# Kernel tuning notes

Measured on AMD Instinct MI355X. Metric: run time of the kernel, lower is better.

The kernel has to match this reference:

```python
import math
import jax, jax.numpy as jnp
import numpy as np

NUM_HEADS = 8
HEAD_DIM = 64


def setup_inputs() -> dict:
    key = jax.random.key(0)
    k1, k2, k3, k4 = jax.random.split(key, 4)
    C = 256
    E = NUM_HEADS * HEAD_DIM  # 512
    x = jax.random.normal(k1, (4, C, 48, 48), dtype=jnp.float32)
    Wqkv = jax.random.normal(k2, (3 * E, C), dtype=jnp.float32) * (1.0 / math.sqrt(C))
    Wout = jax.random.normal(k3, (C, E), dtype=jnp.float32) * (1.0 / math.sqrt(E))
    bout = jax.random.normal(k4, (C,), dtype=jnp.float32) * 0.01
    return {"x": x, "Wqkv": Wqkv, "Wout": Wout, "bout": bout}


def reference(x, Wqkv, Wout, bout):
    b, c, H, W = x.shape
    nh, hd = NUM_HEADS, HEAD_DIM
    N = H * W
    scale = 1.0 / math.sqrt(hd)
    # 1x1 conv (no bias) == channel matmul
    qkv = jnp.einsum('bcxy,oc->boxy', x, Wqkv)            # [b, 3*nh*hd, H, W]
    qkv = qkv.reshape(b, 3, nh, hd, N)                    # channel split order: (k, h, d)
    q, k, v = qkv[:, 0], qkv[:, 1], qkv[:, 2]             # each [b, nh, hd, N]
    att = jnp.einsum('bhdi,bhdj->bhij', q, k) * scale     # [b, nh, N, N]
    att = jax.nn.softmax(att, axis=-1)                    # stable (max-subtract inside)
    out = jnp.einsum('bhij,bhdj->bhid', att, v)           # [b, nh, N, hd]
    out = out.transpose(0, 1, 3, 2).reshape(b, nh * hd, H, W)  # 'b h (x y) d -> b (h d) x y'
    # 1x1 conv with bias
    return jnp.einsum('bexy,ce->bcxy', out, Wout) + bout[None, :, None, None]
```

## Files before the change

### kernel.cpp

```cpp
#include <hip/hip_runtime.h>

typedef __attribute__((ext_vector_type(8))) __bf16 bf16x8;
typedef __attribute__((ext_vector_type(16))) float f32x16;
typedef __attribute__((ext_vector_type(4))) float f32x4;
typedef __attribute__((ext_vector_type(4))) unsigned short us4;

__device__ __forceinline__ unsigned short f2bf(float f) {
  __bf16 h = (__bf16)f;
  return __builtin_bit_cast(unsigned short, h);
}
__device__ __forceinline__ unsigned pack2bf(float lo, float hi) {
  return (unsigned)f2bf(lo) | ((unsigned)f2bf(hi) << 16);
}

#define GLL(src, dst)                                                            \
  __builtin_amdgcn_global_load_lds((const __attribute__((address_space(1))) void*)(src), \
                                   (__attribute__((address_space(3))) void*)(dst), 16, 0, 0)

__device__ __forceinline__ void stage_chunks(const unsigned short* g, int ld,
                                             unsigned short* lds, int rows, int tid) {
  int total = rows * 8;
  for (int c0 = 0; c0 < total; c0 += 256) {
    int c = c0 + tid;
    int row = c >> 3, kc = c & 7;
    const unsigned short* src = g + (size_t)row * ld + ((kc ^ (row & 7)) << 3);
    unsigned short* dst = lds + (size_t)(c0 + (tid & 192)) * 8;
    GLL(src, dst);
  }
}

__device__ __forceinline__ bf16x8 frag(const unsigned short* lds, int row, int kc) {
  return *(const bf16x8*)(lds + row * 64 + ((kc ^ (row & 7)) << 3));
}


__global__ void k_cvt(const float* __restrict__ in, unsigned short* __restrict__ outp, int n) {
  int i = (blockIdx.x * 256 + threadIdx.x) * 4;
  if (i + 3 < n) {
    f32x4 v = *(const f32x4*)(in + i);
    us4 o;
#pragma unroll
    for (int k = 0; k < 4; k++) o[k] = f2bf(v[k]);
    *(us4*)(outp + i) = o;
  }
}

__global__ __launch_bounds__(256) void k_xpose(const float* __restrict__ x,
                                               unsigned short* __restrict__ xT) {
  __shared__ float t[32][33];
  int tid = threadIdx.x;
  int col = tid & 31, rowb = tid >> 5;
  int nt = blockIdx.x * 32, ct = blockIdx.y * 32, b = blockIdx.z;
  const float* src = x + ((size_t)b * 256 + ct) * 2304 + nt;
#pragma unroll
  for (int rr = 0; rr < 32; rr += 8) t[rowb + rr][col] = src[(size_t)(rowb + rr) * 2304 + col];
  __syncthreads();
  unsigned short* dst = xT + ((size_t)b * 2304 + nt) * 256 + ct;
#pragma unroll
  for (int rr = 0; rr < 32; rr += 8) dst[(size_t)(rowb + rr) * 256 + col] = f2bf(t[col][rowb + rr]);
}

__global__ __launch_bounds__(256, 2) void k_gemm_qkv(
    const unsigned short* __restrict__ W, const unsigned short* __restrict__ xT,
    unsigned short* __restrict__ qT, unsigned short* __restrict__ kT,
    unsigned short* __restrict__ vv) {
  __shared__ unsigned short As[128 * 64];
  __shared__ unsigned short Bs[128 * 64];
  int tid = threadIdx.x, lane = tid & 63, wid = tid >> 6;
  int m0 = blockIdx.x * 128, n0 = blockIdx.y * 128, b = blockIdx.z;
  const unsigned short* Ag = W + (size_t)m0 * 256;
  const unsigned short* Bg = xT + ((size_t)b * 2304 + n0) * 256;
  int wm = (wid >> 1) * 64, wn = (wid & 1) * 64;
  f32x4 acc[4][4] = {};
  for (int kt = 0; kt < 256; kt += 64) {
    __syncthreads();
    stage_chunks(Ag + kt, 256, As, 128, tid);
    stage_chunks(Bg + kt, 256, Bs, 128, tid);
    __syncthreads();
#pragma unroll
    for (int kk = 0; kk < 2; kk++) {
      bf16x8 af[4], bf[4];
#pragma unroll
      for (int i = 0; i < 4; i++) af[i] = frag(As, wm + i * 16 + (lane & 15), kk * 4 + (lane >> 4));
#pragma unroll
      for (int j = 0; j < 4; j++) bf[j] = frag(Bs, wn + j * 16 + (lane & 15), kk * 4 + (lane >> 4));
#pragma unroll
      for (int i = 0; i < 4; i++)
#pragma unroll
        for (int j = 0; j < 4; j++)
          acc[i][j] = __builtin_amdgcn_mfma_f32_16x16x32_bf16(af[i], bf[j], acc[i][j], 0, 0, 0);
    }
  }
#pragma unroll
  for (int i = 0; i < 4; i++) {
    int o = m0 + wm + i * 16 + ((lane >> 4) << 2);
    int which = o >> 9, h = (o >> 6) & 7, d0 = o & 63;
#pragma unroll
    for (int j = 0; j < 4; j++) {
      int n = n0 + wn + j * 16 + (lane & 15);
      if (which == 2) {
#pragma unroll
        for (int jj = 0; jj < 4; jj++)
          vv[((size_t)(b * 8 + h) * 64 + d0 + jj) * 2304 + n] = f2bf(acc[i][j][jj]);
      } else {
        float sc = which ? 1.0f : 0.18033688011112042f;
        us4 pk;
#pragma unroll
        for (int jj = 0; jj < 4; jj++) pk[jj] = f2bf(acc[i][j][jj] * sc);
        unsigned short* dst = (which ? kT : qT) + ((size_t)(b * 8 + h) * 2304 + n) * 64 + d0;
        *(us4*)dst = pk;
      }
    }
  }
}

__global__ __launch_bounds__(256, 4) void k_attn(
    const unsigned short* __restrict__ qT, const unsigned short* __restrict__ kT,
    const unsigned short* __restrict__ vv, unsigned short* __restrict__ o2T) {
  __shared__ unsigned short L[2][2][4096];
  int tid = threadIdx.x, lane = tid & 63;
  int wid = tid >> 6, rh = wid & 1, jh = wid >> 1;
  int il = lane & 31, g = lane >> 5;
  int lin = blockIdx.x;
  int xcd = lin & 7, idx = lin >> 3;
  int bh = xcd * 4 + idx / 36;
  int i0 = (idx % 36) * 64;
  const unsigned short* kT_bh = kT + (size_t)bh * 2304 * 64;
  const unsigned short* vv_bh = vv + (size_t)bh * 64 * 2304;
  const unsigned short* qrow = qT + ((size_t)bh * 2304 + i0 + rh * 32 + il) * 64;
  bf16x8 qf[4];
#pragma unroll
  for (int ks = 0; ks < 4; ks++) qf[ks] = *(const bf16x8*)(qrow + (ks * 2 + g) * 8);

  int cA = tid, cB = tid + 256;
  int rA = cA >> 3, rB = cB >> 3;
  unsigned swA = (unsigned)((((cA & 7) ^ ((rA + (rA >> 3)) & 7))) << 3);
  unsigned swB = (unsigned)((((cB & 7) ^ ((rB + (rB >> 3)) & 7))) << 3);
  unsigned oKA = rA * 64 + swA, oKB = rB * 64 + swB;
  unsigned oVA = rA * 2304 + swA, oVB = rB * 2304 + swB;
  int db = (tid & 192) * 8;
  unsigned short* dKA = &L[0][0][db];
  unsigned short* dKB = &L[0][0][2048 + db];
  unsigned short* dVA = &L[0][1][db];
  unsigned short* dVB = &L[0][1][2048 + db];

#define STAGE(boff)                          \
  do {                                       \
    GLL(kT_bh + oKA, dKA + (boff));          \
    GLL(kT_bh + oKB, dKB + (boff));          \
    GLL(vv_bh + oVA, dVA + (boff));          \
    GLL(vv_bh + oVB, dVB + (boff));          \
    oKA += 4096; oKB += 4096; oVA += 64; oVB += 64; \
  } while (0)

  const unsigned short* fK[4];
  const unsigned short* fV[4];
#pragma unroll
  for (int ks = 0; ks < 4; ks++) {
    int cs = ks * 2 + g;
    int row = jh * 32 + il;
    fK[ks] = &L[0][0][row * 64 + (((cs ^ ((row + (row >> 3)) & 7))) << 3)];
  }
#pragma unroll
  for (int ks = 0; ks < 2; ks++)
#pragma unroll
    for (int dblk = 0; dblk < 2; dblk++) {
      int cs = jh * 4 + ks * 2 + g;
      int row = dblk * 32 + il;
      fV[ks * 2 + dblk] = &L[0][1][row * 64 + (((cs ^ ((row + (row >> 3)) & 7))) << 3)];
    }

  float lrun = 0.f;
  f32x16 O0 = {}, O1 = {};

#define COMP(boff)                                                                      \
  do {                                                                                  \
    bf16x8 kf[4];                                                                       \
    _Pragma("unroll") for (int q = 0; q < 4; q++) kf[q] = *(const bf16x8*)(fK[q] + (boff)); \
    f32x16 S0 = {};                                                                     \
    __builtin_amdgcn_s_setprio(1);                                                      \
    _Pragma("unroll") for (int ks = 0; ks < 4; ks++)                                    \
      S0 = __builtin_amdgcn_mfma_f32_32x32x16_bf16(kf[ks], qf[ks], S0, 0, 0, 0);        \
    __builtin_amdgcn_s_setprio(0);                                                      \
    float a16[16];                                                                      \
    _Pragma("unroll") for (int r = 0; r < 16; r++) {                                    \
      S0[r] = __builtin_amdgcn_exp2f(S0[r]);                                            \
      a16[r] = S0[r];                                                                   \
    }                                                                                   \
    _Pragma("unroll") for (int s = 8; s >= 1; s >>= 1)                                  \
        _Pragma("unroll") for (int r = 0; r < 8; r++) if (r < s) a16[r] += a16[r + s];  \
    lrun += a16[0];                                                                     \
    unsigned w[8];                                                                      \
    _Pragma("unroll") for (int m = 0; m < 8; m++) w[m] = pack2bf(S0[2 * m], S0[2 * m + 1]); \
    bf16x8 vf[4];                                                                       \
    _Pragma("unroll") for (int q = 0; q < 4; q++) vf[q] = *(const bf16x8*)(fV[q] + (boff)); \
    __builtin_amdgcn_s_setprio(1);                                                      \
    _Pragma("unroll") for (int ks = 0; ks < 2; ks++) {                                  \
      unsigned A0 = w[4 * ks], A1 = w[4 * ks + 1], B0 = w[4 * ks + 2], B1 = w[4 * ks + 3]; \
      unsigned send0 = g ? A0 : B0, send1 = g ? A1 : B1;                                \
      unsigned pw0 = __shfl_xor(send0, 32), pw1 = __shfl_xor(send1, 32);                \
      union { unsigned u[4]; bf16x8 v; } F;                                             \
      F.u[0] = g ? pw0 : A0;                                                            \
      F.u[1] = g ? pw1 : A1;                                                            \
      F.u[2] = g ? B0 : pw0;                                                            \
      F.u[3] = g ? B1 : pw1;                                                            \
      O0 = __builtin_amdgcn_mfma_f32_32x32x16_bf16(vf[ks * 2 + 0], F.v, O0, 0, 0, 0);   \
      O1 = __builtin_amdgcn_mfma_f32_32x32x16_bf16(vf[ks * 2 + 1], F.v, O1, 0, 0, 0);   \
    }                                                                                   \
    __builtin_amdgcn_s_setprio(0);                                                      \
  } while (0)

  STAGE(0);
  __syncthreads();
#pragma unroll 1
  for (int it = 0; it < 18; it++) {
    STAGE(8192);
    COMP(0);
    __syncthreads();
    if (it < 17) STAGE(0);
    COMP(8192);
    __syncthreads();
  }
#undef STAGE
#undef COMP

  lrun += __shfl_xor(lrun, 32);
  float* sm = (float*)&L[0][0][0];
  float* ml = (float*)&L[1][0][0];
  if (jh == 1) {
#pragma unroll
    for (int r = 0; r < 16; r++) {
      sm[(rh * 32 + r) * 64 + lane] = O0[r];
      sm[(rh * 32 + 16 + r) * 64 + lane] = O1[r];
    }
    if (!g) ml[rh * 32 + il] = lrun;
  }
  __syncthreads();
  if (jh == 0) {
    float rl = 1.0f / (lrun + ml[rh * 32 + il]);
    int b = bh >> 3, h = bh & 7;
    unsigned short* dst = o2T + ((size_t)b * 2304 + (i0 + rh * 32 + il)) * 512 + h * 64;
#pragma unroll
    for (int dt = 0; dt < 2; dt++) {
#pragma unroll
      for (int u = 0; u < 4; u++) {
        us4 pk;
#pragma unroll
        for (int v = 0; v < 4; v++) {
          int r = 4 * u + v;
          float own = dt ? O1[r] : O0[r];
          float oth = sm[(rh * 32 + dt * 16 + r) * 64 + lane];
          pk[v] = f2bf((own + oth) * rl);
        }
        *(us4*)(dst + dt * 32 + 8 * u + 4 * g) = pk;
      }
    }
  }
}

__global__ __launch_bounds__(256, 2) void k_gemm_out(
    const unsigned short* __restrict__ Wo, const unsigned short* __restrict__ o2T,
    const float* __restrict__ bout, float* __restrict__ out) {
  __shared__ unsigned short As[128 * 64];
  __shared__ unsigned short Bs[128 * 64];
  int tid = threadIdx.x, lane = tid & 63, wid = tid >> 6;
  int m0 = blockIdx.x * 128, n0 = blockIdx.y * 128, b = blockIdx.z;
  const unsigned short* Ag = Wo + (size_t)m0 * 512;
  const unsigned short* Bg = o2T + ((size_t)b * 2304 + n0) * 512;
  int wm = (wid >> 1) * 64, wn = (wid & 1) * 64;
  f32x4 acc[4][4] = {};
  for (int kt = 0; kt < 512; kt += 64) {
    __syncthreads();
    stage_chunks(Ag + kt, 512, As, 128, tid);
    stage_chunks(Bg + kt, 512, Bs, 128, tid);
    __syncthreads();
#pragma unroll
    for (int kk = 0; kk < 2; kk++) {
      bf16x8 af[4], bf[4];
#pragma unroll
      for (int i = 0; i < 4; i++) af[i] = frag(As, wm + i * 16 + (lane & 15), kk * 4 + (lane >> 4));
#pragma unroll
      for (int j = 0; j < 4; j++) bf[j] = frag(Bs, wn + j * 16 + (lane & 15), kk * 4 + (lane >> 4));
#pragma unroll
      for (int i = 0; i < 4; i++)
#pragma unroll
        for (int j = 0; j < 4; j++)
          acc[i][j] = __builtin_amdgcn_mfma_f32_16x16x32_bf16(af[i], bf[j], acc[i][j], 0, 0, 0);
    }
  }
#pragma unroll
  for (int i = 0; i < 4; i++) {
    int c = m0 + wm + i * 16 + ((lane >> 4) << 2);
#pragma unroll
    for (int j = 0; j < 4; j++) {
      int n = n0 + wn + j * 16 + (lane & 15);
#pragma unroll
      for (int jj = 0; jj < 4; jj++)
        out[((size_t)b * 256 + c + jj) * 2304 + n] = acc[i][j][jj] + bout[c + jj];
    }
  }
}

extern "C" void kernel_launch(void* const* d_in, const int* in_sizes, int n_in,
                              void* d_out, int out_size, void* d_ws, size_t ws_size,
                              hipStream_t stream) {
  const float* x = (const float*)d_in[0];
  const float* Wqkv = (const float*)d_in[1];
  const float* Wout = (const float*)d_in[2];
  const float* bout = (const float*)d_in[3];
  float* out = (float*)d_out;
  char* ws = (char*)d_ws;
  unsigned short* Wqkv_bf = (unsigned short*)(ws + 0);
  unsigned short* Wout_bf = (unsigned short*)(ws + 786432);
  unsigned short* xT      = (unsigned short*)(ws + 1048576);
  unsigned short* qT      = (unsigned short*)(ws + 5767168);
  unsigned short* kT      = (unsigned short*)(ws + 15204352);
  unsigned short* vv      = (unsigned short*)(ws + 24641536);
  unsigned short* o2T     = (unsigned short*)(ws + 34078720);

  k_cvt<<<dim3(384), dim3(256), 0, stream>>>(Wqkv, Wqkv_bf, 1536 * 256);
  k_cvt<<<dim3(128), dim3(256), 0, stream>>>(Wout, Wout_bf, 256 * 512);
  k_xpose<<<dim3(72, 8, 4), dim3(256), 0, stream>>>(x, xT);
  k_gemm_qkv<<<dim3(12, 18, 4), dim3(256), 0, stream>>>(Wqkv_bf, xT, qT, kT, vv);
  k_attn<<<dim3(1152), dim3(256), 0, stream>>>(qT, kT, vv, o2T);
  k_gemm_out<<<dim3(2, 18, 4), dim3(256), 0, stream>>>(Wout_bf, o2T, bout, out);
}
```

Baseline: 112.6 us.

## Double attention query tile per block to share K/V staging across more waves

The attention kernel now runs 512-thread blocks that each cover 128 query rows instead of 64. Each K/V tile loaded into LDS is therefore reused by four row-groups, which halves global-to-LDS traffic per query and halves the number of blocks. The per-iteration horizontal reduction of exp values is replaced by per-element accumulators that are reduced once after the loop. The extra accumulators and the tighter launch bound (512 threads, 4 blocks) shrink the register budget per thread, which risks spills or lower effective occupancy.

```diff
diff --git a/kernel.cpp b/kernel.cpp
--- a/kernel.cpp
+++ b/kernel.cpp
@@ -114,17 +114,18 @@
   }
 }
 
-__global__ __launch_bounds__(256, 4) void k_attn(
+__global__ __launch_bounds__(512, 4) void k_attn(
     const unsigned short* __restrict__ qT, const unsigned short* __restrict__ kT,
     const unsigned short* __restrict__ vv, unsigned short* __restrict__ o2T) {
   __shared__ unsigned short L[2][2][4096];
+  __shared__ float ml[128];
   int tid = threadIdx.x, lane = tid & 63;
-  int wid = tid >> 6, rh = wid & 1, jh = wid >> 1;
+  int wid = tid >> 6, rh = wid & 3, jh = wid >> 2;
   int il = lane & 31, g = lane >> 5;
   int lin = blockIdx.x;
   int xcd = lin & 7, idx = lin >> 3;
-  int bh = xcd * 4 + idx / 36;
-  int i0 = (idx % 36) * 64;
+  int bh = xcd * 4 + idx / 18;
+  int i0 = (idx % 18) * 128;
   const unsigned short* kT_bh = kT + (size_t)bh * 2304 * 64;
   const unsigned short* vv_bh = vv + (size_t)bh * 64 * 2304;
   const unsigned short* qrow = qT + ((size_t)bh * 2304 + i0 + rh * 32 + il) * 64;
@@ -132,25 +133,19 @@
 #pragma unroll
   for (int ks = 0; ks < 4; ks++) qf[ks] = *(const bf16x8*)(qrow + (ks * 2 + g) * 8);
 
-  int cA = tid, cB = tid + 256;
-  int rA = cA >> 3, rB = cB >> 3;
-  unsigned swA = (unsigned)((((cA & 7) ^ ((rA + (rA >> 3)) & 7))) << 3);
-  unsigned swB = (unsigned)((((cB & 7) ^ ((rB + (rB >> 3)) & 7))) << 3);
-  unsigned oKA = rA * 64 + swA, oKB = rB * 64 + swB;
-  unsigned oVA = rA * 2304 + swA, oVB = rB * 2304 + swB;
-  int db = (tid & 192) * 8;
-  unsigned short* dKA = &L[0][0][db];
-  unsigned short* dKB = &L[0][0][2048 + db];
-  unsigned short* dVA = &L[0][1][db];
-  unsigned short* dVB = &L[0][1][2048 + db];
-
-#define STAGE(boff)                          \
-  do {                                       \
-    GLL(kT_bh + oKA, dKA + (boff));          \
-    GLL(kT_bh + oKB, dKB + (boff));          \
-    GLL(vv_bh + oVA, dVA + (boff));          \
-    GLL(vv_bh + oVB, dVB + (boff));          \
-    oKA += 4096; oKB += 4096; oVA += 64; oVB += 64; \
+  int srow = tid >> 3, skc = tid & 7;
+  unsigned sw = (unsigned)(((skc ^ ((srow + (srow >> 3)) & 7))) << 3);
+  unsigned oK = srow * 64 + sw;
+  unsigned oV = srow * 2304 + sw;
+  int db = (tid & 448) * 8;
+  unsigned short* dK = &L[0][0][db];
+  unsigned short* dV = &L[0][1][db];
+
+#define STAGE(boff)                   \
+  do {                                \
+    GLL(kT_bh + oK, dK + (boff));     \
+    GLL(vv_bh + oV, dV + (boff));     \
+    oK += 4096; oV += 64;             \
   } while (0)
 
   const unsigned short* fK[4];
@@ -170,7 +165,7 @@
       fV[ks * 2 + dblk] = &L[0][1][row * 64 + (((cs ^ ((row + (row >> 3)) & 7))) << 3)];
     }
 
-  float lrun = 0.f;
+  float a16[16] = {};
   f32x16 O0 = {}, O1 = {};
 
 #define COMP(boff)                                                                      \
@@ -182,14 +177,10 @@
     _Pragma("unroll") for (int ks = 0; ks < 4; ks++)                                    \
       S0 = __builtin_amdgcn_mfma_f32_32x32x16_bf16(kf[ks], qf[ks], S0, 0, 0, 0);        \
     __builtin_amdgcn_s_setprio(0);                                                      \
-    float a16[16];                                                                      \
     _Pragma("unroll") for (int r = 0; r < 16; r++) {                                    \
       S0[r] = __builtin_amdgcn_exp2f(S0[r]);                                            \
-      a16[r] = S0[r];                                                                   \
+      a16[r] += S0[r];                                                                  \
     }                                                                                   \
-    _Pragma("unroll") for (int s = 8; s >= 1; s >>= 1)                                  \
-        _Pragma("unroll") for (int r = 0; r < 8; r++) if (r < s) a16[r] += a16[r + s];  \
-    lrun += a16[0];                                                                     \
     unsigned w[8];                                                                      \
     _Pragma("unroll") for (int m = 0; m < 8; m++) w[m] = pack2bf(S0[2 * m], S0[2 * m + 1]); \
     bf16x8 vf[4];                                                                       \
@@ -224,9 +215,14 @@
 #undef STAGE
 #undef COMP
 
-  lrun += __shfl_xor(lrun, 32);
+#pragma unroll
+  for (int s = 8; s >= 1; s >>= 1)
+#pragma unroll
+    for (int r = 0; r < 8; r++)
+      if (r < s) a16[r] += a16[r + s];
+  float lrun = a16[0] + __shfl_xor(a16[0], 32);
+  __syncthreads();
   float* sm = (float*)&L[0][0][0];
-  float* ml = (float*)&L[1][0][0];
   if (jh == 1) {
 #pragma unroll
     for (int r = 0; r < 16; r++) {
@@ -322,6 +318,6 @@
   k_cvt<<<dim3(128), dim3(256), 0, stream>>>(Wout, Wout_bf, 256 * 512);
   k_xpose<<<dim3(72, 8, 4), dim3(256), 0, stream>>>(x, xT);
   k_gemm_qkv<<<dim3(12, 18, 4), dim3(256), 0, stream>>>(Wqkv_bf, xT, qT, kT, vv);
-  k_attn<<<dim3(1152), dim3(256), 0, stream>>>(qT, kT, vv, o2T);
+  k_attn<<<dim3(576), dim3(512), 0, stream>>>(qT, kT, vv, o2T);
   k_gemm_out<<<dim3(2, 18, 4), dim3(256), 0, stream>>>(Wout_bf, o2T, bout, out);
 }
```

New measurement: 116.7 us. +3.6%, slower.
